# Kernel tuning notes

Hardware: AMD Instinct MI355X
Metric: run time of the kernel (lower is better)

The kernel has to match this reference:

```python
import jax, jax.numpy as jnp
import numpy as np

D_MODEL = 512
H = 8
DEPTH = D_MODEL // H
TOPK = 16
TAU_HID = max(4, D_MODEL // 2)  # 256
TAU_EPS = 1e-6
DT = 1.0
T_SCALAR = 1.0  # default t in call()


def setup_inputs() -> dict:
    key = jax.random.key(0)
    ks = jax.random.split(key, 24)
    B, T = 2, 1024
    D2 = 2 * DEPTH

    def w(k, shape, fan_in):
        return jax.random.normal(k, shape, dtype=jnp.float32) / np.sqrt(fan_in)

    inp = {
        "x": jax.random.normal(ks[0], (B, T, D_MODEL), dtype=jnp.float32),
        "Wq": w(ks[1], (D_MODEL, D_MODEL), D_MODEL), "bq": jnp.zeros((D_MODEL,), jnp.float32),
        "Wk": w(ks[2], (D_MODEL, D_MODEL), D_MODEL), "bk": jnp.zeros((D_MODEL,), jnp.float32),
        "Wv": w(ks[3], (D_MODEL, D_MODEL), D_MODEL), "bv": jnp.zeros((D_MODEL,), jnp.float32),
        "Wo": w(ks[4], (D_MODEL, D_MODEL), D_MODEL), "bo": jnp.zeros((D_MODEL,), jnp.float32),
        "Wpi": w(ks[5], (D2, D_MODEL), D2), "bpi": jnp.zeros((D_MODEL,), jnp.float32),
        "Wpo": w(ks[6], (D_MODEL, 1), D_MODEL), "bpo": jnp.zeros((1,), jnp.float32),
        "Wta": w(ks[7], (D2, 1), D2), "bta": jnp.zeros((1,), jnp.float32),
        "Wtb": w(ks[8], (D2, 1), D2), "btb": jnp.zeros((1,), jnp.float32),
        "Wti": w(ks[9], (D2, TAU_HID), D2), "bti": jnp.zeros((TAU_HID,), jnp.float32),
        "Wto": w(ks[10], (TAU_HID, 1), TAU_HID), "bto": jnp.zeros((1,), jnp.float32),
    }
    return inp


def reference(x, Wq, bq, Wk, bk, Wv, bv, Wo, bo,
              Wpi, bpi, Wpo, bpo, Wta, bta, Wtb, btb, Wti, bti, Wto, bto):
    B, T, _ = x.shape

    def split_heads(z):
        return z.reshape(B, T, H, DEPTH).transpose(0, 2, 1, 3)  # [B,H,T,D]

    qh = split_heads(x @ Wq + bq)
    kh = split_heads(x @ Wk + bk)
    vh = split_heads(x @ Wv + bv)

    # top-k pairwise scores (q @ k^T), select K keys per query
    scores = jnp.einsum('bhqd,bhkd->bhqk', qh, kh)  # [B,H,T,T]
    _, idx = jax.lax.top_k(scores, TOPK)            # [B,H,T,K]

    # gather k and v at top-k indices -> [B,H,T,K,D]
    kg = jnp.take_along_axis(kh[:, :, None, :, :], idx[..., None], axis=3)
    vg = jnp.take_along_axis(vh[:, :, None, :, :], idx[..., None], axis=3)

    # per-pair features [q_i ; k_j] -> [B,H,T,K,2D]
    qt = jnp.broadcast_to(qh[:, :, :, None, :], (B, H, T, TOPK, DEPTH))
    pairs = jnp.concatenate([qt, kg], axis=-1)

    # phi: Dense(d_model) -> Dense(1) -> sigmoid
    phi = jax.nn.sigmoid(((pairs @ Wpi + bpi) @ Wpo + bpo)[..., 0])
    # time interpolation: sigmoid(a*t + b)
    t_a = (pairs @ Wta + bta)[..., 0]
    t_b = (pairs @ Wtb + btb)[..., 0]
    t_interp = jax.nn.sigmoid(t_a * T_SCALAR + t_b)
    # tau: Dense(d_model//2) -> Dense(1) -> softplus + eps
    tau = jax.nn.softplus(((pairs @ Wti + bti) @ Wto + bto)[..., 0]) + TAU_EPS

    # mode == 'exact'
    attn_logits = phi / tau * (1.0 - jnp.exp(-tau * t_interp))
    attn = jax.nn.softmax(attn_logits, axis=-1)  # [B,H,T,K]

    out_h = jnp.einsum('bhqk,bhqkd->bhqd', attn, vg) * DT  # [B,H,T,D]
    combined = out_h.transpose(0, 2, 1, 3).reshape(B, T, D_MODEL)
    return combined @ Wo + bo  # return_sequences=True
```

## Files before the change

kernel.cpp:

```cpp
#include <hip/hip_runtime.h>
#include <math.h>

#define BDIM 2
#define TT 1024
#define NH 8
#define HD 64
#define NTOPK 16
#define NBH 16
#define NTOK 16384

__global__ __launch_bounds__(256) void k_collapse64(
    const float* __restrict__ Wpi, const float* __restrict__ bpi,
    const float* __restrict__ Wpo, const float* __restrict__ bpo,
    const float* __restrict__ Wti, const float* __restrict__ bti,
    const float* __restrict__ Wto, const float* __restrict__ bto,
    double* __restrict__ wphid, double* __restrict__ wtaud,
    double* __restrict__ ccd) {
  int tid = threadIdx.x;
  int blk = blockIdx.x;
  if (blk < 16) {
    int r = blk * 16 + (tid >> 4);
    int l = tid & 15;
    double s = 0.;
    if (r < 128) {
      for (int i = 0; i < 32; ++i)
        s += (double)Wpi[r * 512 + l + 16 * i] * (double)Wpo[l + 16 * i];
    } else {
      int rr = r - 128;
      for (int i = 0; i < 16; ++i)
        s += (double)Wti[rr * 256 + l + 16 * i] * (double)Wto[l + 16 * i];
    }
#pragma unroll
    for (int off = 8; off >= 1; off >>= 1) s += __shfl_xor(s, off, 64);
    if (l == 0) {
      if (r < 128) wphid[r] = s;
      else wtaud[r - 128] = s;
    }
  } else {
    int lane = tid & 63;
    if (tid < 64) {
      double p = 0.;
      for (int c = lane; c < 512; c += 64) p += (double)bpi[c] * (double)Wpo[c];
#pragma unroll
      for (int off = 32; off >= 1; off >>= 1) p += __shfl_xor(p, off, 64);
      if (lane == 0) ccd[0] = p + (double)bpo[0];
    } else if (tid < 128) {
      double p = 0.;
      for (int c = lane; c < 256; c += 64) p += (double)bti[c] * (double)Wto[c];
#pragma unroll
      for (int off = 32; off >= 1; off >>= 1) p += __shfl_xor(p, off, 64);
      if (lane == 0) ccd[1] = p + (double)bto[0];
    }
  }
}

__device__ __forceinline__ void gemm_body(
    const float* __restrict__ A, const float* __restrict__ W,
    const float* __restrict__ bias, float* __restrict__ out,
    int bm, int bn, int mode) {
  __shared__ float As[16][64];
  __shared__ float Bs[16][64];
  const int tid = threadIdx.x;
  const int tx = tid & 15;
  const int ty = tid >> 4;
  const int lr = tid >> 2;
  const int lc = (tid & 3) << 2;
  float acc[4][4] = {{0.f, 0.f, 0.f, 0.f}};
  for (int k0 = 0; k0 < 512; k0 += 16) {
    float4 av = *(const float4*)&A[(bm + lr) * 512 + k0 + lc];
    As[lc + 0][lr] = av.x;
    As[lc + 1][lr] = av.y;
    As[lc + 2][lr] = av.z;
    As[lc + 3][lr] = av.w;
    *(float4*)&Bs[ty][tx << 2] = *(const float4*)&W[(k0 + ty) * 512 + bn + (tx << 2)];
    __syncthreads();
#pragma unroll
    for (int kk = 0; kk < 16; ++kk) {
      float a0 = As[kk][ty * 4 + 0];
      float a1 = As[kk][ty * 4 + 1];
      float a2 = As[kk][ty * 4 + 2];
      float a3 = As[kk][ty * 4 + 3];
      float4 b = *(const float4*)&Bs[kk][tx << 2];
      acc[0][0] = fmaf(a0, b.x, acc[0][0]);
      acc[0][1] = fmaf(a0, b.y, acc[0][1]);
      acc[0][2] = fmaf(a0, b.z, acc[0][2]);
      acc[0][3] = fmaf(a0, b.w, acc[0][3]);
      acc[1][0] = fmaf(a1, b.x, acc[1][0]);
      acc[1][1] = fmaf(a1, b.y, acc[1][1]);
      acc[1][2] = fmaf(a1, b.z, acc[1][2]);
      acc[1][3] = fmaf(a1, b.w, acc[1][3]);
      acc[2][0] = fmaf(a2, b.x, acc[2][0]);
      acc[2][1] = fmaf(a2, b.y, acc[2][1]);
      acc[2][2] = fmaf(a2, b.z, acc[2][2]);
      acc[2][3] = fmaf(a2, b.w, acc[2][3]);
      acc[3][0] = fmaf(a3, b.x, acc[3][0]);
      acc[3][1] = fmaf(a3, b.y, acc[3][1]);
      acc[3][2] = fmaf(a3, b.z, acc[3][2]);
      acc[3][3] = fmaf(a3, b.w, acc[3][3]);
    }
    __syncthreads();
  }
#pragma unroll
  for (int i = 0; i < 4; ++i) {
    int row = bm + ty * 4 + i;
    float4 r;
    r.x = acc[i][0] + bias[bn + tx * 4 + 0];
    r.y = acc[i][1] + bias[bn + tx * 4 + 1];
    r.z = acc[i][2] + bias[bn + tx * 4 + 2];
    r.w = acc[i][3] + bias[bn + tx * 4 + 3];
    if (mode == 0) {
      *(float4*)&out[row * 512 + bn + tx * 4] = r;
    } else {
      int bb = row >> 10;
      int tt2 = row & 1023;
      int head = bn >> 6;
      *(float4*)&out[(((bb * NH + head) * TT + tt2) << 6) + tx * 4] = r;
    }
  }
}

__global__ __launch_bounds__(256) void k_gemm(
    const float* __restrict__ A, const float* __restrict__ W,
    const float* __restrict__ bias, float* __restrict__ out, int mode) {
  gemm_body(A, W, bias, out, blockIdx.y * 64, blockIdx.x * 64, mode);
}

__global__ __launch_bounds__(256) void k_gemm_qkv(
    const float* __restrict__ A,
    const float* __restrict__ Wq, const float* __restrict__ bq,
    const float* __restrict__ Wk, const float* __restrict__ bk,
    const float* __restrict__ Wv, const float* __restrict__ bv,
    float* __restrict__ Qf, float* __restrict__ Kf, float* __restrict__ Vf) {
  int which = blockIdx.x >> 3;
  int bn = (blockIdx.x & 7) * 64;
  const float* W = (which == 0) ? Wq : (which == 1) ? Wk : Wv;
  const float* b = (which == 0) ? bq : (which == 1) ? bk : bv;
  float* out = (which == 0) ? Qf : (which == 1) ? Kf : Vf;
  gemm_body(A, W, b, out, blockIdx.y * 64, bn, 1);
}

__global__ __launch_bounds__(256) void k_tokscal64(
    const float* __restrict__ Qg, const float* __restrict__ Kg,
    const double* __restrict__ wphid, const float* __restrict__ Wta,
    const float* __restrict__ Wtb, const double* __restrict__ wtaud,
    double4* __restrict__ sqd4, double4* __restrict__ skd4) {
  __shared__ double wp[128], wa[128], wb[128], wt[128];
  int tid = threadIdx.x;
  if (tid < 128) {
    wp[tid] = wphid[tid];
    wa[tid] = (double)Wta[tid];
    wb[tid] = (double)Wtb[tid];
    wt[tid] = wtaud[tid];
  }
  __syncthreads();
  int tok = blockIdx.x * 256 + tid;
  const float* qr = Qg + (size_t)tok * 64;
  const float* kr = Kg + (size_t)tok * 64;
  double sp = 0., sa = 0., sb = 0., st = 0.;
  double kp = 0., ka = 0., kb2 = 0., kt = 0.;
#pragma unroll
  for (int d = 0; d < 64; ++d) {
    double q = (double)qr[d];
    double k = (double)kr[d];
    sp += q * wp[d];
    sa += q * wa[d];
    sb += q * wb[d];
    st += q * wt[d];
    kp += k * wp[64 + d];
    ka += k * wa[64 + d];
    kb2 += k * wb[64 + d];
    kt += k * wt[64 + d];
  }
  sqd4[tok] = make_double4(sp, sa, sb, st);
  skd4[tok] = make_double4(kp, ka, kb2, kt);
}

__global__ __launch_bounds__(256) void k_trans(
    const float* __restrict__ Kf, float* __restrict__ Kt) {
  __shared__ float tile[64][65];
  const int kt0 = blockIdx.x * 64;
  const int bh = blockIdx.y;
  const int t = threadIdx.x;
  const int rr = t >> 4;
  const int d4 = (t & 15) << 2;
#pragma unroll
  for (int i = 0; i < 4; ++i) {
    int row = i * 16 + rr;
    float4 v = *(const float4*)&Kf[((size_t)(bh * TT + kt0 + row)) * 64 + d4];
    tile[row][d4 + 0] = v.x;
    tile[row][d4 + 1] = v.y;
    tile[row][d4 + 2] = v.z;
    tile[row][d4 + 3] = v.w;
  }
  __syncthreads();
#pragma unroll
  for (int i = 0; i < 4; ++i) {
    int d = i * 16 + rr;
    int k4 = (t & 15) << 2;
    float4 v;
    v.x = tile[k4 + 0][d];
    v.y = tile[k4 + 1][d];
    v.z = tile[k4 + 2][d];
    v.w = tile[k4 + 3][d];
    *(float4*)&Kt[((size_t)(bh * 64 + d)) * 1024 + kt0 + k4] = v;
  }
}

__global__ __launch_bounds__(256) void k_score(
    const float* __restrict__ Qf, const float* __restrict__ Kt,
    float* __restrict__ Sc) {
  __shared__ float As[16][132];
  __shared__ float Bs[16][64];
  const int bn = blockIdx.x * 64;
  const int bm = blockIdx.y * 128;
  const int bh = blockIdx.z;
  const float* A = Qf + (size_t)bh * (TT * 64);
  const float* W = Kt + (size_t)bh * (64 * 1024);
  float* out = Sc + (size_t)bh * (TT * 1024);
  const int tid = threadIdx.x;
  const int tx = tid & 15;
  const int ty = tid >> 4;
  const int lr = tid >> 2;
  const int lc = (tid & 3) << 2;
  float acc[8][4];
#pragma unroll
  for (int i = 0; i < 8; ++i)
#pragma unroll
    for (int j = 0; j < 4; ++j) acc[i][j] = 0.f;
  for (int k0 = 0; k0 < 64; k0 += 16) {
#pragma unroll
    for (int h = 0; h < 2; ++h) {
      int row = h * 64 + lr;
      float4 av = *(const float4*)&A[(size_t)(bm + row) * 64 + k0 + lc];
      As[lc + 0][row] = av.x;
      As[lc + 1][row] = av.y;
      As[lc + 2][row] = av.z;
      As[lc + 3][row] = av.w;
    }
    *(float4*)&Bs[ty][tx << 2] = *(const float4*)&W[(size_t)(k0 + ty) * 1024 + bn + (tx << 2)];
    __syncthreads();
#pragma unroll
    for (int kk = 0; kk < 16; ++kk) {
      float4 alo = *(const float4*)&As[kk][ty * 8];
      float4 ahi = *(const float4*)&As[kk][ty * 8 + 4];
      float4 b = *(const float4*)&Bs[kk][tx << 2];
      acc[0][0] = fmaf(alo.x, b.x, acc[0][0]);
      acc[0][1] = fmaf(alo.x, b.y, acc[0][1]);
      acc[0][2] = fmaf(alo.x, b.z, acc[0][2]);
      acc[0][3] = fmaf(alo.x, b.w, acc[0][3]);
      acc[1][0] = fmaf(alo.y, b.x, acc[1][0]);
      acc[1][1] = fmaf(alo.y, b.y, acc[1][1]);
      acc[1][2] = fmaf(alo.y, b.z, acc[1][2]);
      acc[1][3] = fmaf(alo.y, b.w, acc[1][3]);
      acc[2][0] = fmaf(alo.z, b.x, acc[2][0]);
      acc[2][1] = fmaf(alo.z, b.y, acc[2][1]);
      acc[2][2] = fmaf(alo.z, b.z, acc[2][2]);
      acc[2][3] = fmaf(alo.z, b.w, acc[2][3]);
      acc[3][0] = fmaf(alo.w, b.x, acc[3][0]);
      acc[3][1] = fmaf(alo.w, b.y, acc[3][1]);
      acc[3][2] = fmaf(alo.w, b.z, acc[3][2]);
      acc[3][3] = fmaf(alo.w, b.w, acc[3][3]);
      acc[4][0] = fmaf(ahi.x, b.x, acc[4][0]);
      acc[4][1] = fmaf(ahi.x, b.y, acc[4][1]);
      acc[4][2] = fmaf(ahi.x, b.z, acc[4][2]);
      acc[4][3] = fmaf(ahi.x, b.w, acc[4][3]);
      acc[5][0] = fmaf(ahi.y, b.x, acc[5][0]);
      acc[5][1] = fmaf(ahi.y, b.y, acc[5][1]);
      acc[5][2] = fmaf(ahi.y, b.z, acc[5][2]);
      acc[5][3] = fmaf(ahi.y, b.w, acc[5][3]);
      acc[6][0] = fmaf(ahi.z, b.x, acc[6][0]);
      acc[6][1] = fmaf(ahi.z, b.y, acc[6][1]);
      acc[6][2] = fmaf(ahi.z, b.z, acc[6][2]);
      acc[6][3] = fmaf(ahi.z, b.w, acc[6][3]);
      acc[7][0] = fmaf(ahi.w, b.x, acc[7][0]);
      acc[7][1] = fmaf(ahi.w, b.y, acc[7][1]);
      acc[7][2] = fmaf(ahi.w, b.z, acc[7][2]);
      acc[7][3] = fmaf(ahi.w, b.w, acc[7][3]);
    }
    __syncthreads();
  }
#pragma unroll
  for (int i = 0; i < 8; ++i) {
    float4 r = make_float4(acc[i][0], acc[i][1], acc[i][2], acc[i][3]);
    *(float4*)&out[(size_t)(bm + ty * 8 + i) * 1024 + bn + (tx << 2)] = r;
  }
}

__global__ __launch_bounds__(256) void k_topk(
    const float* __restrict__ Sc, const float* __restrict__ Vg,
    const double4* __restrict__ sqd4, const double4* __restrict__ skd4,
    const double* __restrict__ ccd, const float* __restrict__ btaP,
    const float* __restrict__ btbP, float* __restrict__ C) {
  const int tid = threadIdx.x;
  const int lane = tid & 63;
  const int wv = tid >> 6;
  const int qg = blockIdx.x * 4 + wv;
  const int bh = qg >> 10;
  const int qa = qg & 1023;
  const int bb = bh >> 3;
  const int hh = bh & 7;
  const float* rowp = Sc + (size_t)qg * 1024;
  const float* Vbh = Vg + (size_t)bh * (TT * 64);

  float v[16];
#pragma unroll
  for (int jj = 0; jj < 16; ++jj) v[jj] = rowp[jj * 64 + lane];
  float gv[4];
  int gj[4];
#pragma unroll
  for (int g = 0; g < 4; ++g) {
    gv[g] = v[4 * g];
    gj[g] = 4 * g;
#pragma unroll
    for (int e = 1; e < 4; ++e) {
      if (v[4 * g + e] > gv[g]) { gv[g] = v[4 * g + e]; gj[g] = 4 * g + e; }
    }
  }
  int myk = 0;
#pragma unroll 1
  for (int it = 0; it < NTOPK; ++it) {
    float bvv = gv[0];
    int bjj = gj[0];
#pragma unroll
    for (int g = 1; g < 4; ++g) {
      if (gv[g] > bvv) { bvv = gv[g]; bjj = gj[g]; }
    }
    int bj = bjj * 64 + lane;
#pragma unroll
    for (int off = 32; off >= 1; off >>= 1) {
      float ov = __shfl_xor(bvv, off, 64);
      int oj = __shfl_xor(bj, off, 64);
      if (ov > bvv || (ov == bvv && oj < bj)) { bvv = ov; bj = oj; }
    }
    if (lane == it) myk = bj;
    int owner = bj & 63;
    int slot = bj >> 6;
    if (lane == owner) {
#pragma unroll
      for (int jj = 0; jj < 16; ++jj)
        if (jj == slot) v[jj] = -INFINITY;
      int g2 = slot >> 2;
#pragma unroll
      for (int g = 0; g < 4; ++g) {
        if (g == g2) {
          float ngv = v[4 * g];
          int ngj = 4 * g;
#pragma unroll
          for (int e = 1; e < 4; ++e) {
            if (v[4 * g + e] > ngv) { ngv = v[4 * g + e]; ngj = 4 * g + e; }
          }
          gv[g] = ngv;
          gj[g] = ngj;
        }
      }
    }
  }
  const double cphi = ccd[0];
  const double ctau = ccd[1];
  const double bta0 = (double)btaP[0];
  const double btb0 = (double)btbP[0];
  double4 sq = sqd4[qg];
  double logit = -INFINITY;
  if (lane < 16) {
    double4 sk = skd4[bh * TT + myk];
    double phi = 1.0 / (1.0 + exp(-(sq.x + sk.x + cphi)));
    double ta = sq.y + sk.y + bta0;
    double tb = sq.z + sk.z + btb0;
    double ti = 1.0 / (1.0 + exp(-(ta * 1.0 + tb)));
    double tl = sq.w + sk.w + ctau;
    double tau = fmax(tl, 0.0) + log1p(exp(-fabs(tl))) + 1e-6;
    logit = phi / tau * (1.0 - exp(-tau * ti));
  }
  double m = logit;
#pragma unroll
  for (int off = 8; off >= 1; off >>= 1) {
    double om = __shfl_xor(m, off, 64);
    m = fmax(m, om);
  }
  double e = (lane < 16) ? exp(logit - m) : 0.0;
  double ssum = e;
#pragma unroll
  for (int off = 8; off >= 1; off >>= 1) ssum += __shfl_xor(ssum, off, 64);
  double w = e / ssum;
  double outv = 0.0;
#pragma unroll
  for (int k2 = 0; k2 < NTOPK; ++k2) {
    double wk = __shfl(w, k2, 64);
    int ik = __shfl(myk, k2, 64);
    outv += wk * (double)Vbh[(size_t)ik * 64 + lane];
  }
  C[(bb * TT + qa) * 512 + hh * 64 + lane] = (float)outv;
}

__global__ __launch_bounds__(256) void k_attn(
    const float* __restrict__ Qg, const float* __restrict__ Kg,
    const float* __restrict__ Vg, const double4* __restrict__ sqd4,
    const double4* __restrict__ skd4, const double* __restrict__ ccd,
    const float* __restrict__ btaP, const float* __restrict__ btbP,
    float* __restrict__ C) {
  __shared__ float qs[8][64];
  __shared__ float sc[8][1024];
  const int bh = blockIdx.y;
  const int q0 = blockIdx.x * 8;
  const int tid = threadIdx.x;
  const int lane = tid & 63;
  const int wv = tid >> 6;
  if (tid < 128) {
    int q = tid >> 4, d4 = (tid & 15) << 2;
    *(float4*)&qs[q][d4] = *(const float4*)&Qg[(size_t)(bh * TT + q0 + q) * 64 + d4];
  }
  __syncthreads();
#pragma unroll 1
  for (int c = 0; c < 4; ++c) {
    const int kb = (c * 4 + wv) * 64;
    const float* krow = &Kg[(size_t)(bh * TT + kb + lane) * 64];
    float4 kr[16];
#pragma unroll
    for (int i = 0; i < 16; ++i) kr[i] = *(const float4*)&krow[i * 4];
#pragma unroll
    for (int q = 0; q < 8; ++q) {
      float s = 0.f;
#pragma unroll
      for (int i = 0; i < 16; ++i) {
        float4 q4 = *(const float4*)&qs[q][i * 4];
        s = fmaf(q4.x, kr[i].x, s);
        s = fmaf(q4.y, kr[i].y, s);
        s = fmaf(q4.z, kr[i].z, s);
        s = fmaf(q4.w, kr[i].w, s);
      }
      sc[q][kb + lane] = s;
    }
  }
  __syncthreads();
  const double cphi = ccd[0];
  const double ctau = ccd[1];
  const double bta0 = (double)btaP[0];
  const double btb0 = (double)btbP[0];
  const int bb = bh >> 3;
  const int hh = bh & 7;
  const float* Vbh = Vg + (size_t)bh * (TT * 64);
#pragma unroll 1
  for (int qq = 0; qq < 2; ++qq) {
    const int ql = wv * 2 + qq;
    const int qa = q0 + ql;
    const float* rowp = &sc[ql][0];
    float v[16];
#pragma unroll
    for (int jj = 0; jj < 16; ++jj) v[jj] = rowp[jj * 64 + lane];
    float gv[4];
    int gj[4];
#pragma unroll
    for (int g = 0; g < 4; ++g) {
      gv[g] = v[4 * g];
      gj[g] = 4 * g;
#pragma unroll
      for (int e = 1; e < 4; ++e) {
        if (v[4 * g + e] > gv[g]) { gv[g] = v[4 * g + e]; gj[g] = 4 * g + e; }
      }
    }
    int myk = 0;
#pragma unroll 1
    for (int it = 0; it < NTOPK; ++it) {
      float bvv = gv[0];
      int bjj = gj[0];
#pragma unroll
      for (int g = 1; g < 4; ++g) {
        if (gv[g] > bvv) { bvv = gv[g]; bjj = gj[g]; }
      }
      int bj = bjj * 64 + lane;
#pragma unroll
      for (int off = 32; off >= 1; off >>= 1) {
        float ov = __shfl_xor(bvv, off, 64);
        int oj = __shfl_xor(bj, off, 64);
        if (ov > bvv || (ov == bvv && oj < bj)) { bvv = ov; bj = oj; }
      }
      if (lane == it) myk = bj;
      int owner = bj & 63;
      int slot = bj >> 6;
      if (lane == owner) {
#pragma unroll
        for (int jj = 0; jj < 16; ++jj)
          if (jj == slot) v[jj] = -INFINITY;
        int g2 = slot >> 2;
#pragma unroll
        for (int g = 0; g < 4; ++g) {
          if (g == g2) {
            float ngv = v[4 * g];
            int ngj = 4 * g;
#pragma unroll
            for (int e = 1; e < 4; ++e) {
              if (v[4 * g + e] > ngv) { ngv = v[4 * g + e]; ngj = 4 * g + e; }
            }
            gv[g] = ngv;
            gj[g] = ngj;
          }
        }
      }
    }
    double4 sq = sqd4[bh * TT + qa];
    double logit = -INFINITY;
    if (lane < 16) {
      double4 sk = skd4[bh * TT + myk];
      double phi = 1.0 / (1.0 + exp(-(sq.x + sk.x + cphi)));
      double ta = sq.y + sk.y + bta0;
      double tb = sq.z + sk.z + btb0;
      double ti = 1.0 / (1.0 + exp(-(ta * 1.0 + tb)));
      double tl = sq.w + sk.w + ctau;
      double tau = fmax(tl, 0.0) + log1p(exp(-fabs(tl))) + 1e-6;
      logit = phi / tau * (1.0 - exp(-tau * ti));
    }
    double m = logit;
#pragma unroll
    for (int off = 8; off >= 1; off >>= 1) {
      double om = __shfl_xor(m, off, 64);
      m = fmax(m, om);
    }
    double e = (lane < 16) ? exp(logit - m) : 0.0;
    double ssum = e;
#pragma unroll
    for (int off = 8; off >= 1; off >>= 1) ssum += __shfl_xor(ssum, off, 64);
    double w = e / ssum;
    double outv = 0.0;
#pragma unroll
    for (int k2 = 0; k2 < NTOPK; ++k2) {
      double wk = __shfl(w, k2, 64);
      int ik = __shfl(myk, k2, 64);
      outv += wk * (double)Vbh[(size_t)ik * 64 + lane];
    }
    C[(bb * TT + qa) * 512 + hh * 64 + lane] = (float)outv;
  }
}

extern "C" void kernel_launch(void* const* d_in, const int* in_sizes, int n_in,
                              void* d_out, int out_size, void* d_ws, size_t ws_size,
                              hipStream_t stream) {
  (void)in_sizes; (void)n_in; (void)out_size;
  const float* x   = (const float*)d_in[0];
  const float* Wq  = (const float*)d_in[1];
  const float* bq  = (const float*)d_in[2];
  const float* Wk  = (const float*)d_in[3];
  const float* bk  = (const float*)d_in[4];
  const float* Wv  = (const float*)d_in[5];
  const float* bv  = (const float*)d_in[6];
  const float* Wo  = (const float*)d_in[7];
  const float* bo  = (const float*)d_in[8];
  const float* Wpi = (const float*)d_in[9];
  const float* bpi = (const float*)d_in[10];
  const float* Wpo = (const float*)d_in[11];
  const float* bpo = (const float*)d_in[12];
  const float* Wta = (const float*)d_in[13];
  const float* bta = (const float*)d_in[14];
  const float* Wtb = (const float*)d_in[15];
  const float* btb = (const float*)d_in[16];
  const float* Wti = (const float*)d_in[17];
  const float* bti = (const float*)d_in[18];
  const float* Wto = (const float*)d_in[19];
  const float* bto = (const float*)d_in[20];

  double* wsd = (double*)d_ws;
  double4* sqd4 = (double4*)wsd;
  double4* skd4 = (double4*)(wsd + 65536);
  double* wphid = wsd + 131072;
  double* wtaud = wsd + 131200;
  double* ccd   = wsd + 131328;
  float* fs = (float*)(wsd + 131332);
  float* Qf = fs;
  float* Kf = fs + 1048576;
  float* Vf = fs + 2097152;
  float* Cf = fs + 3145728;
  float* Kt = fs + 4194304;
  float* Sc = fs + 5242880;
  const size_t need = (size_t)131332 * 8 + (size_t)(5242880 + 16777216) * 4;

  hipLaunchKernelGGL(k_collapse64, dim3(17), dim3(256), 0, stream,
                     Wpi, bpi, Wpo, bpo, Wti, bti, Wto, bto, wphid, wtaud, ccd);
  hipLaunchKernelGGL(k_gemm_qkv, dim3(24, 32), dim3(256), 0, stream,
                     x, Wq, bq, Wk, bk, Wv, bv, Qf, Kf, Vf);
  hipLaunchKernelGGL(k_tokscal64, dim3(NTOK / 256), dim3(256), 0, stream,
                     Qf, Kf, wphid, Wta, Wtb, wtaud, sqd4, skd4);
  if (ws_size >= need) {
    hipLaunchKernelGGL(k_trans, dim3(16, 16), dim3(256), 0, stream, Kf, Kt);
    hipLaunchKernelGGL(k_score, dim3(16, 8, 16), dim3(256), 0, stream, Qf, Kt, Sc);
    hipLaunchKernelGGL(k_topk, dim3(NTOK / 4), dim3(256), 0, stream,
                       Sc, Vf, sqd4, skd4, ccd, bta, btb, Cf);
  } else {
    hipLaunchKernelGGL(k_attn, dim3(TT / 8, NBH), dim3(256), 0, stream,
                       Qf, Kf, Vf, sqd4, skd4, ccd, bta, btb, Cf);
  }
  hipLaunchKernelGGL(k_gemm, dim3(8, 32), dim3(256), 0, stream,
                     Cf, Wo, bo, (float*)d_out, 0);
}
```

Before: 301.0 us.

## Vectorize loads, widen score K-tile, and switch top-k epilogue to float

The linear GEMM now reads its A fragment as a single float4 LDS load. The score GEMM stages 32-wide K tiles instead of 16, which halves the number of barriers. The top-k kernel loads score rows as float4, using a new per-lane index mapping with matching owner and slot decoding. The logit, softmax and weighted-V epilogue moves from double to float with fast exp intrinsics, which cuts costly FP64 work but reduces accuracy.

```diff
diff --git a/kernel.cpp b/kernel.cpp
--- a/kernel.cpp
+++ b/kernel.cpp
@@ -76,27 +76,24 @@
     __syncthreads();
 #pragma unroll
     for (int kk = 0; kk < 16; ++kk) {
-      float a0 = As[kk][ty * 4 + 0];
-      float a1 = As[kk][ty * 4 + 1];
-      float a2 = As[kk][ty * 4 + 2];
-      float a3 = As[kk][ty * 4 + 3];
+      float4 a = *(const float4*)&As[kk][ty * 4];
       float4 b = *(const float4*)&Bs[kk][tx << 2];
-      acc[0][0] = fmaf(a0, b.x, acc[0][0]);
-      acc[0][1] = fmaf(a0, b.y, acc[0][1]);
-      acc[0][2] = fmaf(a0, b.z, acc[0][2]);
-      acc[0][3] = fmaf(a0, b.w, acc[0][3]);
-      acc[1][0] = fmaf(a1, b.x, acc[1][0]);
-      acc[1][1] = fmaf(a1, b.y, acc[1][1]);
-      acc[1][2] = fmaf(a1, b.z, acc[1][2]);
-      acc[1][3] = fmaf(a1, b.w, acc[1][3]);
-      acc[2][0] = fmaf(a2, b.x, acc[2][0]);
-      acc[2][1] = fmaf(a2, b.y, acc[2][1]);
-      acc[2][2] = fmaf(a2, b.z, acc[2][2]);
-      acc[2][3] = fmaf(a2, b.w, acc[2][3]);
-      acc[3][0] = fmaf(a3, b.x, acc[3][0]);
-      acc[3][1] = fmaf(a3, b.y, acc[3][1]);
-      acc[3][2] = fmaf(a3, b.z, acc[3][2]);
-      acc[3][3] = fmaf(a3, b.w, acc[3][3]);
+      acc[0][0] = fmaf(a.x, b.x, acc[0][0]);
+      acc[0][1] = fmaf(a.x, b.y, acc[0][1]);
+      acc[0][2] = fmaf(a.x, b.z, acc[0][2]);
+      acc[0][3] = fmaf(a.x, b.w, acc[0][3]);
+      acc[1][0] = fmaf(a.y, b.x, acc[1][0]);
+      acc[1][1] = fmaf(a.y, b.y, acc[1][1]);
+      acc[1][2] = fmaf(a.y, b.z, acc[1][2]);
+      acc[1][3] = fmaf(a.y, b.w, acc[1][3]);
+      acc[2][0] = fmaf(a.z, b.x, acc[2][0]);
+      acc[2][1] = fmaf(a.z, b.y, acc[2][1]);
+      acc[2][2] = fmaf(a.z, b.z, acc[2][2]);
+      acc[2][3] = fmaf(a.z, b.w, acc[2][3]);
+      acc[3][0] = fmaf(a.w, b.x, acc[3][0]);
+      acc[3][1] = fmaf(a.w, b.y, acc[3][1]);
+      acc[3][2] = fmaf(a.w, b.z, acc[3][2]);
+      acc[3][3] = fmaf(a.w, b.w, acc[3][3]);
     }
     __syncthreads();
   }
@@ -209,8 +206,8 @@
 __global__ __launch_bounds__(256) void k_score(
     const float* __restrict__ Qf, const float* __restrict__ Kt,
     float* __restrict__ Sc) {
-  __shared__ float As[16][132];
-  __shared__ float Bs[16][64];
+  __shared__ float As[32][132];
+  __shared__ float Bs[32][64];
   const int bn = blockIdx.x * 64;
   const int bm = blockIdx.y * 128;
   const int bh = blockIdx.z;
@@ -220,27 +217,33 @@
   const int tid = threadIdx.x;
   const int tx = tid & 15;
   const int ty = tid >> 4;
-  const int lr = tid >> 2;
-  const int lc = (tid & 3) << 2;
   float acc[8][4];
 #pragma unroll
   for (int i = 0; i < 8; ++i)
 #pragma unroll
     for (int j = 0; j < 4; ++j) acc[i][j] = 0.f;
-  for (int k0 = 0; k0 < 64; k0 += 16) {
-#pragma unroll
-    for (int h = 0; h < 2; ++h) {
-      int row = h * 64 + lr;
-      float4 av = *(const float4*)&A[(size_t)(bm + row) * 64 + k0 + lc];
-      As[lc + 0][row] = av.x;
-      As[lc + 1][row] = av.y;
-      As[lc + 2][row] = av.z;
-      As[lc + 3][row] = av.w;
-    }
-    *(float4*)&Bs[ty][tx << 2] = *(const float4*)&W[(size_t)(k0 + ty) * 1024 + bn + (tx << 2)];
+  for (int k0 = 0; k0 < 64; k0 += 32) {
+#pragma unroll
+    for (int i = 0; i < 4; ++i) {
+      int idx = i * 256 + tid;
+      int row = idx >> 3;
+      int c4 = (idx & 7) << 2;
+      float4 av = *(const float4*)&A[(size_t)(bm + row) * 64 + k0 + c4];
+      As[c4 + 0][row] = av.x;
+      As[c4 + 1][row] = av.y;
+      As[c4 + 2][row] = av.z;
+      As[c4 + 3][row] = av.w;
+    }
+#pragma unroll
+    for (int i = 0; i < 2; ++i) {
+      int idx = i * 256 + tid;
+      int br = idx >> 4;
+      int bc = (idx & 15) << 2;
+      *(float4*)&Bs[br][bc] = *(const float4*)&W[(size_t)(k0 + br) * 1024 + bn + bc];
+    }
     __syncthreads();
 #pragma unroll
-    for (int kk = 0; kk < 16; ++kk) {
+    for (int kk = 0; kk < 32; ++kk) {
       float4 alo = *(const float4*)&As[kk][ty * 8];
       float4 ahi = *(const float4*)&As[kk][ty * 8 + 4];
       float4 b = *(const float4*)&Bs[kk][tx << 2];
@@ -304,7 +307,13 @@
 
   float v[16];
 #pragma unroll
-  for (int jj = 0; jj < 16; ++jj) v[jj] = rowp[jj * 64 + lane];
+  for (int j4 = 0; j4 < 4; ++j4) {
+    float4 t = *(const float4*)&rowp[j4 * 256 + lane * 4];
+    v[j4 * 4 + 0] = t.x;
+    v[j4 * 4 + 1] = t.y;
+    v[j4 * 4 + 2] = t.z;
+    v[j4 * 4 + 3] = t.w;
+  }
   float gv[4];
   int gj[4];
 #pragma unroll
@@ -325,7 +334,7 @@
     for (int g = 1; g < 4; ++g) {
       if (gv[g] > bvv) { bvv = gv[g]; bjj = gj[g]; }
     }
-    int bj = bjj * 64 + lane;
+    int bj = ((bjj >> 2) << 8) + (lane << 2) + (bjj & 3);
 #pragma unroll
     for (int off = 32; off >= 1; off >>= 1) {
       float ov = __shfl_xor(bvv, off, 64);
@@ -333,8 +342,8 @@
       if (ov > bvv || (ov == bvv && oj < bj)) { bvv = ov; bj = oj; }
     }
     if (lane == it) myk = bj;
-    int owner = bj & 63;
-    int slot = bj >> 6;
+    int owner = (bj >> 2) & 63;
+    int slot = (((bj >> 8) << 2)) | (bj & 3);
     if (lane == owner) {
 #pragma unroll
       for (int jj = 0; jj < 16; ++jj)
@@ -360,36 +369,34 @@
   const double bta0 = (double)btaP[0];
   const double btb0 = (double)btbP[0];
   double4 sq = sqd4[qg];
-  double logit = -INFINITY;
+  float logit = -INFINITY;
   if (lane < 16) {
     double4 sk = skd4[bh * TT + myk];
-    double phi = 1.0 / (1.0 + exp(-(sq.x + sk.x + cphi)));
-    double ta = sq.y + sk.y + bta0;
-    double tb = sq.z + sk.z + btb0;
-    double ti = 1.0 / (1.0 + exp(-(ta * 1.0 + tb)));
-    double tl = sq.w + sk.w + ctau;
-    double tau = fmax(tl, 0.0) + log1p(exp(-fabs(tl))) + 1e-6;
-    logit = phi / tau * (1.0 - exp(-tau * ti));
-  }
-  double m = logit;
-#pragma unroll
-  for (int off = 8; off >= 1; off >>= 1) {
-    double om = __shfl_xor(m, off, 64);
-    m = fmax(m, om);
-  }
-  double e = (lane < 16) ? exp(logit - m) : 0.0;
-  double ssum = e;
+    float xs = (float)(sq.x + sk.x + cphi);
+    float ta = (float)(sq.y + sk.y + bta0);
+    float tb = (float)(sq.z + sk.z + btb0);
+    float tl = (float)(sq.w + sk.w + ctau);
+    float phi = 1.f / (1.f + __expf(-xs));
+    float ti = 1.f / (1.f + __expf(-(ta + tb)));
+    float tau = fmaxf(tl, 0.f) + log1pf(__expf(-fabsf(tl))) + 1e-6f;
+    logit = phi / tau * (1.f - __expf(-tau * ti));
+  }
+  float m = logit;
+#pragma unroll
+  for (int off = 8; off >= 1; off >>= 1) m = fmaxf(m, __shfl_xor(m, off, 64));
+  float e = (lane < 16) ? __expf(logit - m) : 0.f;
+  float ssum = e;
 #pragma unroll
   for (int off = 8; off >= 1; off >>= 1) ssum += __shfl_xor(ssum, off, 64);
-  double w = e / ssum;
-  double outv = 0.0;
+  float w = e / ssum;
+  float outv = 0.f;
 #pragma unroll
   for (int k2 = 0; k2 < NTOPK; ++k2) {
-    double wk = __shfl(w, k2, 64);
+    float wk = __shfl(w, k2, 64);
     int ik = __shfl(myk, k2, 64);
-    outv += wk * (double)Vbh[(size_t)ik * 64 + lane];
-  }
-  C[(bb * TT + qa) * 512 + hh * 64 + lane] = (float)outv;
+    outv = fmaf(wk, Vbh[(size_t)ik * 64 + lane], outv);
+  }
+  C[(bb * TT + qa) * 512 + hh * 64 + lane] = outv;
 }
 
 __global__ __launch_bounds__(256) void k_attn(
```

Result: faster. 276.0 us (-8.3%).
